# Performance work log

Hardware: AMD Instinct MI355X
Metric: run time of the kernel (lower is better)

Reference implementation:

```python
import math
import jax, jax.numpy as jnp
import numpy as np

B, C, D = 4, 1024, 2048
N_EXP, TOP_K, CAP_F = 8, 2, 1.25


def setup_inputs() -> dict:
    key = jax.random.key(0)
    k1, k2, k3, k4 = jax.random.split(key, 4)
    x = jax.random.normal(k1, (B, C, D), dtype=jnp.float32)
    noise = jax.random.normal(k2, (B, C, N_EXP), dtype=jnp.float32)
    w_g = jax.random.normal(k3, (N_EXP, D), dtype=jnp.float32) * 0.02
    w_noise = jax.random.normal(k4, (N_EXP, D), dtype=jnp.float32) * 0.02
    return {"x": x, "noise": noise, "w_g": w_g, "w_noise": w_noise}


def reference(x, noise, w_g, w_noise):
    b, c, d = x.shape
    T = b * c  # num_tokens
    E, k = w_g.shape[0], TOP_K

    # gating logits with noisy top-k (noise eps passed in explicitly)
    logits = jnp.einsum('bcd,ed->bce', x, w_g)
    logits = logits + jax.nn.softplus(jnp.einsum('bcd,ed->bce', x, w_noise)) * noise

    top_vals, top_idx = jax.lax.top_k(logits, k)  # (B,C,k)

    # scatter top-k logits into -inf tensor then softmax == mask non-topk to -inf
    onehot_k = jax.nn.one_hot(top_idx, E, dtype=jnp.int32)  # (B,C,k,E)
    topk_mask = onehot_k.sum(axis=-2) > 0                   # (B,C,E)
    router_probs = jax.nn.softmax(jnp.where(topk_mask, logits, -jnp.inf), axis=-1)

    cap = math.floor(k * CAP_F * T / E)
    cap += cap % 2

    # (k, T, E) expert assignment mask
    exp_mask = onehot_k.reshape(T, k, E).transpose(1, 0, 2)
    # position-in-expert rank via cumulative sum over (k*T, E)
    exp_rank = jnp.cumsum(exp_mask.reshape(k * T, E), axis=0) - 1
    exp_rank = exp_rank.reshape(k, T, E)
    exp_mask = exp_mask * (exp_rank < cap).astype(jnp.int32)
    rank = jnp.sum(exp_mask * exp_rank, axis=-1)  # (k, T) int

    probs_flat = router_probs.reshape(T, E)[None]          # (1,T,E)
    w = exp_mask.astype(x.dtype) * probs_flat              # (k,T,E)
    rank_oh = jax.nn.one_hot(rank, cap, dtype=x.dtype)     # (k,T,cap)
    # combine weights: (T, E, cap)
    exp_weights = jnp.einsum('kte,ktc->tec', w, rank_oh)
    exp_mask_out = exp_weights != 0                        # bool (T,E,cap)

    x_flat = x.reshape(T, d)
    # dense one-hot dispatch matmul: (E, cap, T) @ (T, d)
    expert_batches = jnp.einsum('tec,td->ecd', exp_mask_out.astype(x.dtype), x_flat)
    return exp_weights, exp_mask_out, expert_batches
```

## Files before the change

### kernel.cpp

```cpp
#include <hip/hip_runtime.h>

#define T_TOKENS 4096
#define D_DIM    2048
#define NEXP     8
#define CAP      1280
#define NSLOTS   (NEXP * CAP)

typedef float f32x4 __attribute__((ext_vector_type(4)));

__global__ void gating_kernel(const float* __restrict__ x,
                              const float* __restrict__ noise,
                              const float* __restrict__ w_g,
                              const float* __restrict__ w_noise,
                              int*   __restrict__ top_idx,
                              float* __restrict__ top_prob)
{
    const int wave = threadIdx.x >> 6;
    const int lane = threadIdx.x & 63;
    const int t = blockIdx.x * 4 + wave;
    if (t >= T_TOKENS) return;

    const f32x4* xv = reinterpret_cast<const f32x4*>(x + (size_t)t * D_DIM);

    float acc[16];
#pragma unroll
    for (int j = 0; j < 16; ++j) acc[j] = 0.f;

#pragma unroll
    for (int it = 0; it < 8; ++it) {
        const int c = it * 64 + lane;
        const f32x4 xval = xv[c];
#pragma unroll
        for (int e = 0; e < NEXP; ++e) {
            const f32x4 g = reinterpret_cast<const f32x4*>(w_g + (size_t)e * D_DIM)[c];
            acc[e] += xval.x * g.x + xval.y * g.y + xval.z * g.z + xval.w * g.w;
            const f32x4 n = reinterpret_cast<const f32x4*>(w_noise + (size_t)e * D_DIM)[c];
            acc[8 + e] += xval.x * n.x + xval.y * n.y + xval.z * n.z + xval.w * n.w;
        }
    }

#pragma unroll
    for (int j = 0; j < 16; ++j) {
        float v = acc[j];
#pragma unroll
        for (int off = 32; off > 0; off >>= 1) v += __shfl_down(v, off, 64);
        acc[j] = v;
    }

    if (lane == 0) {
        float logit[NEXP];
#pragma unroll
        for (int e = 0; e < NEXP; ++e) {
            const float z = acc[8 + e];
            const float sp = fmaxf(z, 0.f) + log1pf(expf(-fabsf(z)));
            logit[e] = acc[e] + sp * noise[(size_t)t * NEXP + e];
        }
        int i0 = 0; float v0 = logit[0];
#pragma unroll
        for (int e = 1; e < NEXP; ++e) {
            if (logit[e] > v0) { v0 = logit[e]; i0 = e; }
        }
        int i1 = -1; float v1 = -3.402823466e38f;
#pragma unroll
        for (int e = 0; e < NEXP; ++e) {
            if (e != i0 && logit[e] > v1) { v1 = logit[e]; i1 = e; }
        }
        const float e1  = expf(v1 - v0);
        const float inv = 1.f / (1.f + e1);
        top_idx[t]            = i0;
        top_idx[T_TOKENS + t] = i1;
        top_prob[t]            = inv;
        top_prob[T_TOKENS + t] = e1 * inv;
    }
}

__global__ void scan_kernel(const int* __restrict__ top_idx,
                            int* __restrict__ rank,
                            int* __restrict__ slot_token)
{
    __shared__ int sidx[2 * T_TOKENS];
    for (int i = threadIdx.x; i < 2 * T_TOKENS; i += blockDim.x)
        sidx[i] = top_idx[i];
    __syncthreads();

    const int e    = threadIdx.x >> 6;
    const int lane = threadIdx.x & 63;

    int base = 0;
    for (int chunk = 0; chunk < (2 * T_TOKENS) / 64; ++chunk) {
        const int i = chunk * 64 + lane;
        const bool match = (sidx[i] == e);
        const unsigned long long m = __ballot(match);
        if (match) {
            const int r = base + __popcll(m & ((1ull << lane) - 1ull));
            const bool keep = (r < CAP);
            rank[i] = keep ? r : -1;
            if (keep) slot_token[e * CAP + r] = i;
        }
        base += __popcll(m);
    }
}

__global__ void weights_kernel(const int*   __restrict__ top_idx,
                               const float* __restrict__ top_prob,
                               const int*   __restrict__ rank,
                               float* __restrict__ exp_weights,
                               float* __restrict__ exp_mask)
{
    const int t  = blockIdx.x;
    const int e0 = top_idx[t];
    const int e1 = top_idx[T_TOKENS + t];
    const int r0 = rank[t];
    const int r1 = rank[T_TOKENS + t];
    const float w0 = top_prob[t];
    const float w1 = top_prob[T_TOKENS + t];

    const int p0 = (r0 >= 0) ? (e0 * CAP + r0) : -1;
    const int p1 = (r1 >= 0) ? (e1 * CAP + r1) : -1;
    const float m0 = (w0 != 0.f) ? 1.f : 0.f;
    const float m1 = (w1 != 0.f) ? 1.f : 0.f;

    f32x4* wout = reinterpret_cast<f32x4*>(exp_weights + (size_t)t * NSLOTS);
    f32x4* mout = reinterpret_cast<f32x4*>(exp_mask    + (size_t)t * NSLOTS);

#pragma unroll
    for (int f = threadIdx.x; f < NSLOTS / 4; f += 256) {
        const int b = 4 * f;
        f32x4 wv, mv;
        wv.x = (b     == p0) ? w0 : (b     == p1) ? w1 : 0.f;
        wv.y = (b + 1 == p0) ? w0 : (b + 1 == p1) ? w1 : 0.f;
        wv.z = (b + 2 == p0) ? w0 : (b + 2 == p1) ? w1 : 0.f;
        wv.w = (b + 3 == p0) ? w0 : (b + 3 == p1) ? w1 : 0.f;
        mv.x = (b     == p0) ? m0 : (b     == p1) ? m1 : 0.f;
        mv.y = (b + 1 == p0) ? m0 : (b + 1 == p1) ? m1 : 0.f;
        mv.z = (b + 2 == p0) ? m0 : (b + 2 == p1) ? m1 : 0.f;
        mv.w = (b + 3 == p0) ? m0 : (b + 3 == p1) ? m1 : 0.f;
        __builtin_nontemporal_store(wv, wout + f);
        __builtin_nontemporal_store(mv, mout + f);
    }
}

__global__ void batches_kernel(const float* __restrict__ x,
                               const int*   __restrict__ slot_token,
                               float* __restrict__ expert_batches)
{
    const int slot = blockIdx.x;
    const int i = slot_token[slot];
    f32x4* dst = reinterpret_cast<f32x4*>(expert_batches + (size_t)slot * D_DIM);

    if (i >= 0) {
        const int t = i & (T_TOKENS - 1);
        const f32x4* src = reinterpret_cast<const f32x4*>(x + (size_t)t * D_DIM);
#pragma unroll
        for (int c = threadIdx.x; c < D_DIM / 4; c += 256)
            __builtin_nontemporal_store(src[c], dst + c);
    } else {
        const f32x4 z = {0.f, 0.f, 0.f, 0.f};
#pragma unroll
        for (int c = threadIdx.x; c < D_DIM / 4; c += 256)
            __builtin_nontemporal_store(z, dst + c);
    }
}

extern "C" void kernel_launch(void* const* d_in, const int* in_sizes, int n_in,
                              void* d_out, int out_size, void* d_ws, size_t ws_size,
                              hipStream_t stream)
{
    const float* x       = (const float*)d_in[0];
    const float* noise   = (const float*)d_in[1];
    const float* w_g     = (const float*)d_in[2];
    const float* w_noise = (const float*)d_in[3];

    float* out = (float*)d_out;
    const size_t n_ew = (size_t)T_TOKENS * NEXP * CAP;
    float* exp_weights    = out;
    float* exp_mask       = out + n_ew;
    float* expert_batches = out + 2 * n_ew;

    int*   top_idx    = (int*)d_ws;
    float* top_prob   = (float*)((char*)d_ws + 2 * T_TOKENS * 4);
    int*   rank       = (int*)((char*)d_ws + 4 * T_TOKENS * 4);
    int*   slot_token = (int*)((char*)d_ws + 6 * T_TOKENS * 4);

    (void)hipMemsetAsync(slot_token, 0xFF, NSLOTS * sizeof(int), stream);

    gating_kernel<<<T_TOKENS / 4, 256, 0, stream>>>(x, noise, w_g, w_noise,
                                                    top_idx, top_prob);
    scan_kernel<<<1, 512, 0, stream>>>(top_idx, rank, slot_token);
    weights_kernel<<<T_TOKENS, 256, 0, stream>>>(top_idx, top_prob, rank,
                                                 exp_weights, exp_mask);
    batches_kernel<<<NSLOTS, 256, 0, stream>>>(x, slot_token, expert_batches);
}
```

Baseline: 141.2 us.

## Parallelize scan across experts and fuse weight and batch writers

The rank scan now runs one block per expert instead of a single block. Within each block, a two-pass per-wave count and prefix replaces the serial 128-chunk loop. The slot_token memset moves into the scan kernel, and the weights and batches kernels merge into one launch that splits work by block index. The aim is to remove a serial single-block bottleneck and two launches, at the cost of each block reloading the full index array.

Measured after the change: 121.2 us. -14.2%, faster.

```diff
diff --git a/kernel.cpp b/kernel.cpp
--- a/kernel.cpp
+++ b/kernel.cpp
@@ -79,16 +79,34 @@
                             int* __restrict__ slot_token)
 {
     __shared__ int sidx[2 * T_TOKENS];
-    for (int i = threadIdx.x; i < 2 * T_TOKENS; i += blockDim.x)
+    __shared__ int scnt[8];
+
+    const int e    = blockIdx.x;
+    const int w    = threadIdx.x >> 6;
+    const int lane = threadIdx.x & 63;
+
+    for (int i = threadIdx.x; i < 2 * T_TOKENS; i += 512)
         sidx[i] = top_idx[i];
+    for (int r = threadIdx.x; r < CAP; r += 512)
+        slot_token[e * CAP + r] = -1;
     __syncthreads();
 
-    const int e    = threadIdx.x >> 6;
-    const int lane = threadIdx.x & 63;
+    int cnt = 0;
+#pragma unroll
+    for (int c = 0; c < 16; ++c) {
+        const int i = (w * 16 + c) * 64 + lane;
+        cnt += __popcll(__ballot(sidx[i] == e));
+    }
+    if (lane == 0) scnt[w] = cnt;
+    __syncthreads();
 
     int base = 0;
-    for (int chunk = 0; chunk < (2 * T_TOKENS) / 64; ++chunk) {
-        const int i = chunk * 64 + lane;
+#pragma unroll
+    for (int j = 0; j < 8; ++j) if (j < w) base += scnt[j];
+
+#pragma unroll
+    for (int c = 0; c < 16; ++c) {
+        const int i = (w * 16 + c) * 64 + lane;
         const bool match = (sidx[i] == e);
         const unsigned long long m = __ballot(match);
         if (match) {
@@ -101,64 +119,66 @@
     }
 }
 
-__global__ void weights_kernel(const int*   __restrict__ top_idx,
-                               const float* __restrict__ top_prob,
-                               const int*   __restrict__ rank,
-                               float* __restrict__ exp_weights,
-                               float* __restrict__ exp_mask)
-{
-    const int t  = blockIdx.x;
-    const int e0 = top_idx[t];
-    const int e1 = top_idx[T_TOKENS + t];
-    const int r0 = rank[t];
-    const int r1 = rank[T_TOKENS + t];
-    const float w0 = top_prob[t];
-    const float w1 = top_prob[T_TOKENS + t];
-
-    const int p0 = (r0 >= 0) ? (e0 * CAP + r0) : -1;
-    const int p1 = (r1 >= 0) ? (e1 * CAP + r1) : -1;
-    const float m0 = (w0 != 0.f) ? 1.f : 0.f;
-    const float m1 = (w1 != 0.f) ? 1.f : 0.f;
-
-    f32x4* wout = reinterpret_cast<f32x4*>(exp_weights + (size_t)t * NSLOTS);
-    f32x4* mout = reinterpret_cast<f32x4*>(exp_mask    + (size_t)t * NSLOTS);
-
-#pragma unroll
-    for (int f = threadIdx.x; f < NSLOTS / 4; f += 256) {
-        const int b = 4 * f;
-        f32x4 wv, mv;
-        wv.x = (b     == p0) ? w0 : (b     == p1) ? w1 : 0.f;
-        wv.y = (b + 1 == p0) ? w0 : (b + 1 == p1) ? w1 : 0.f;
-        wv.z = (b + 2 == p0) ? w0 : (b + 2 == p1) ? w1 : 0.f;
-        wv.w = (b + 3 == p0) ? w0 : (b + 3 == p1) ? w1 : 0.f;
-        mv.x = (b     == p0) ? m0 : (b     == p1) ? m1 : 0.f;
-        mv.y = (b + 1 == p0) ? m0 : (b + 1 == p1) ? m1 : 0.f;
-        mv.z = (b + 2 == p0) ? m0 : (b + 2 == p1) ? m1 : 0.f;
-        mv.w = (b + 3 == p0) ? m0 : (b + 3 == p1) ? m1 : 0.f;
-        __builtin_nontemporal_store(wv, wout + f);
-        __builtin_nontemporal_store(mv, mout + f);
-    }
-}
-
-__global__ void batches_kernel(const float* __restrict__ x,
-                               const int*   __restrict__ slot_token,
-                               float* __restrict__ expert_batches)
-{
-    const int slot = blockIdx.x;
-    const int i = slot_token[slot];
-    f32x4* dst = reinterpret_cast<f32x4*>(expert_batches + (size_t)slot * D_DIM);
-
-    if (i >= 0) {
-        const int t = i & (T_TOKENS - 1);
-        const f32x4* src = reinterpret_cast<const f32x4*>(x + (size_t)t * D_DIM);
-#pragma unroll
-        for (int c = threadIdx.x; c < D_DIM / 4; c += 256)
-            __builtin_nontemporal_store(src[c], dst + c);
+__global__ void writer_kernel(const float* __restrict__ x,
+                              const int*   __restrict__ top_idx,
+                              const float* __restrict__ top_prob,
+                              const int*   __restrict__ rank,
+                              const int*   __restrict__ slot_token,
+                              float* __restrict__ exp_weights,
+                              float* __restrict__ exp_mask,
+                              float* __restrict__ expert_batches)
+{
+    const int bid = blockIdx.x;
+
+    if (bid < T_TOKENS) {
+        const int t  = bid;
+        const int e0 = top_idx[t];
+        const int e1 = top_idx[T_TOKENS + t];
+        const int r0 = rank[t];
+        const int r1 = rank[T_TOKENS + t];
+        const float w0 = top_prob[t];
+        const float w1 = top_prob[T_TOKENS + t];
+
+        const int p0 = (r0 >= 0) ? (e0 * CAP + r0) : -1;
+        const int p1 = (r1 >= 0) ? (e1 * CAP + r1) : -1;
+        const float m0 = (w0 != 0.f) ? 1.f : 0.f;
+        const float m1 = (w1 != 0.f) ? 1.f : 0.f;
+
+        f32x4* wout = reinterpret_cast<f32x4*>(exp_weights + (size_t)t * NSLOTS);
+        f32x4* mout = reinterpret_cast<f32x4*>(exp_mask    + (size_t)t * NSLOTS);
+
+#pragma unroll
+        for (int f = threadIdx.x; f < NSLOTS / 4; f += 256) {
+            const int b = 4 * f;
+            f32x4 wv, mv;
+            wv.x = (b     == p0) ? w0 : (b     == p1) ? w1 : 0.f;
+            wv.y = (b + 1 == p0) ? w0 : (b + 1 == p1) ? w1 : 0.f;
+            wv.z = (b + 2 == p0) ? w0 : (b + 2 == p1) ? w1 : 0.f;
+            wv.w = (b + 3 == p0) ? w0 : (b + 3 == p1) ? w1 : 0.f;
+            mv.x = (b     == p0) ? m0 : (b     == p1) ? m1 : 0.f;
+            mv.y = (b + 1 == p0) ? m0 : (b + 1 == p1) ? m1 : 0.f;
+            mv.z = (b + 2 == p0) ? m0 : (b + 2 == p1) ? m1 : 0.f;
+            mv.w = (b + 3 == p0) ? m0 : (b + 3 == p1) ? m1 : 0.f;
+            __builtin_nontemporal_store(wv, wout + f);
+            __builtin_nontemporal_store(mv, mout + f);
+        }
     } else {
-        const f32x4 z = {0.f, 0.f, 0.f, 0.f};
-#pragma unroll
-        for (int c = threadIdx.x; c < D_DIM / 4; c += 256)
-            __builtin_nontemporal_store(z, dst + c);
+        const int slot = bid - T_TOKENS;
+        const int i = slot_token[slot];
+        f32x4* dst = reinterpret_cast<f32x4*>(expert_batches + (size_t)slot * D_DIM);
+
+        if (i >= 0) {
+            const int t = i & (T_TOKENS - 1);
+            const f32x4* src = reinterpret_cast<const f32x4*>(x + (size_t)t * D_DIM);
+#pragma unroll
+            for (int c = threadIdx.x; c < D_DIM / 4; c += 256)
+                __builtin_nontemporal_store(src[c], dst + c);
+        } else {
+            const f32x4 z = {0.f, 0.f, 0.f, 0.f};
+#pragma unroll
+            for (int c = threadIdx.x; c < D_DIM / 4; c += 256)
+                __builtin_nontemporal_store(z, dst + c);
+        }
     }
 }
 
@@ -182,12 +202,11 @@
     int*   rank       = (int*)((char*)d_ws + 4 * T_TOKENS * 4);
     int*   slot_token = (int*)((char*)d_ws + 6 * T_TOKENS * 4);
 
-    (void)hipMemsetAsync(slot_token, 0xFF, NSLOTS * sizeof(int), stream);
-
     gating_kernel<<<T_TOKENS / 4, 256, 0, stream>>>(x, noise, w_g, w_noise,
                                                     top_idx, top_prob);
-    scan_kernel<<<1, 512, 0, stream>>>(top_idx, rank, slot_token);
-    weights_kernel<<<T_TOKENS, 256, 0, stream>>>(top_idx, top_prob, rank,
-                                                 exp_weights, exp_mask);
-    batches_kernel<<<NSLOTS, 256, 0, stream>>>(x, slot_token, expert_batches);
-}
+    scan_kernel<<<NEXP, 512, 0, stream>>>(top_idx, rank, slot_token);
+    writer_kernel<<<T_TOKENS + NSLOTS, 256, 0, stream>>>(x, top_idx, top_prob,
+                                                         rank, slot_token,
+                                                         exp_weights, exp_mask,
+                                                         expert_batches);
+}
```
